# Performance work log

Hardware: AMD Instinct MI355X
Metric: run time of the kernel (lower is better)

## Reference

```python
import jax, jax.numpy as jnp
from jax import lax
import numpy as np

KSIZE = 3      # matching patch size
RATE = 2       # down/up-sampling rate
STRIDE = 1
FUSE_K = 3     # diagonal fuse kernel (identity eye(3))
SCALE = 10.0   # softmax_scale


def same_pad(H, k, s):
    out = -(-H // s)
    pt = max((out - 1) * s + k - H, 0)
    return (pt // 2, pt - pt // 2)


def extract_patches(x, k, s):
    # x: [C,H,W] -> patches [L, C, k, k] with TF 'SAME' padding (matches torch extract_image_patches)
    C, H, W = x.shape
    ph = same_pad(H, k, s)
    pw = same_pad(W, k, s)
    xp = jnp.pad(x, ((0, 0), ph, pw))
    Hp, Wp = xp.shape[1], xp.shape[2]
    Ho = (Hp - k) // s + 1
    Wo = (Wp - k) // s + 1
    sl = [xp[:, i:i + (Ho - 1) * s + 1:s, j:j + (Wo - 1) * s + 1:s]
          for i in range(k) for j in range(k)]
    p = jnp.stack(sl, axis=1).reshape(C, k, k, Ho * Wo)  # [C,k,k,L]
    return p.transpose(3, 0, 1, 2)  # [L,C,k,k]


def diag_sum(t, k=FUSE_K):
    # conv2d with eye(k) kernel, SAME padding: out[p,q] = sum_d t[p+d-k//2, q+d-k//2]
    p0 = (k - 1) // 2
    p1 = k - 1 - p0
    tp = jnp.pad(t, ((p0, p1), (p0, p1)))
    H, W = t.shape
    return sum(tp[d:d + H, d:d + W] for d in range(k))


def attend_one(fi, bi):
    # fi, bi: [C,H,W] full resolution
    C, H, W = fi.shape
    kernel = 2 * RATE
    # patches for reconstruction, from full-res background
    raw_w = extract_patches(bi, kernel, RATE * STRIDE)  # [L,C,4,4]
    # nearest downsample by rate for matching
    fs = fi[:, ::RATE, ::RATE]
    bs = bi[:, ::RATE, ::RATE]
    Hs, Ws = fs.shape[1], fs.shape[2]
    L = Hs * Ws
    # matching patches from downscaled background, l2-normalized
    w = extract_patches(bs, KSIZE, STRIDE)  # [L,C,3,3]
    norm = jnp.sqrt(jnp.sum(w * w, axis=(1, 2, 3), keepdims=True))
    wn = (w / jnp.maximum(norm, 1e-4)).reshape(L, -1)  # [L, C*9]
    # correlation conv == im2col matmul: yi[l, q] = <patch_l(b), patch_q(f)>
    fp = extract_patches(fs, KSIZE, 1).reshape(L, -1)  # [HWf, C*9]
    yi = jnp.einsum('lp,qp->lq', wn, fp)  # [HWb, HWf]
    # fuse: propagate scores along diagonals in both orderings
    t = diag_sum(yi)
    t = t.reshape(Hs, Ws, Hs, Ws).transpose(1, 0, 3, 2).reshape(L, L)
    t = diag_sum(t)
    yi = t.reshape(Ws, Hs, Ws, Hs).transpose(1, 0, 3, 2).reshape(L, Hs, Ws)
    # softmax over background-patch axis
    att = jax.nn.softmax(yi * SCALE, axis=0)  # [L,Hs,Ws]
    # conv_transpose2d(att, raw_w, stride=2, padding=1) / 4  via overlap-add
    contrib = jnp.einsum('lhw,lcij->cijhw', att, raw_w)  # [C,4,4,Hs,Ws]
    buf = jnp.zeros((C, 2 * Hs + 2, 2 * Ws + 2), fi.dtype)
    for i in range(kernel):
        for j in range(kernel):
            buf = buf.at[:, i:i + 2 * Hs:2, j:j + 2 * Ws:2].add(contrib[:, i, j])
    return buf[:, 1:2 * Hs + 1, 1:2 * Ws + 1] / 4.0  # [C,H,W]


def conv3x3_elu(x, w, bias):
    y = lax.conv_general_dilated(x, w, (1, 1), [(1, 1), (1, 1)],
                                 dimension_numbers=('NCHW', 'OIHW', 'NCHW'))
    return jax.nn.elu(y + bias[None, :, None, None])


def setup_inputs() -> dict:
    key = jax.random.key(0)
    k1, k2, k3, k4 = jax.random.split(key, 4)
    B, C, H, W = 4, 128, 128, 128
    f = jax.random.normal(k1, (B, C, H, W), jnp.float32)
    b = jax.random.normal(k2, (B, C, H, W), jnp.float32)
    w1 = jax.random.normal(k3, (C, C, 3, 3), jnp.float32) * 0.02
    b1 = jnp.zeros((C,), jnp.float32)
    w2 = jax.random.normal(k4, (C, C, 3, 3), jnp.float32) * 0.02
    b2 = jnp.zeros((C,), jnp.float32)
    return {'f': f, 'b': b, 'w1': w1, 'b1': b1, 'w2': w2, 'b2': b2}


def reference(f, b, w1, b1, w2, b2):
    y = jax.vmap(attend_one)(f, b)  # [B,C,H,W]
    y = conv3x3_elu(y, w1, b1)
    y = conv3x3_elu(y, w2, b2)
    return y
```

## Files before the change

kernel.cpp:

```cpp
#include <hip/hip_runtime.h>
#include <math.h>

using u16 = unsigned short;
using u32 = unsigned int;
typedef _Float16 f16x8 __attribute__((ext_vector_type(8)));
typedef float    f32x4 __attribute__((ext_vector_type(4)));

union F16U { _Float16 h; u16 u; };
__device__ __forceinline__ u16 f2h(float f) { F16U x; x.h = (_Float16)f; return x.u; }
__device__ __forceinline__ float h2f(u16 v) { F16U x; x.u = v; return (float)x.h; }

__device__ __forceinline__ void gl16(const void* g, void* l) {
  __builtin_amdgcn_global_load_lds((const __attribute__((address_space(1))) void*)g,
                                   (__attribute__((address_space(3))) void*)l, 16, 0, 0);
}


__global__ void k_wperm(const float* __restrict__ w, u16* __restrict__ Wp) {
  int idx = blockIdx.x * 256 + threadIdx.x;
  if (idx < 147456) {
    int co = idx / 1152, r = idx - co * 1152, tap = r >> 7, ci = r & 127;
    Wp[idx] = f2h(w[((size_t)co * 128 + ci) * 9 + tap]);
  }
}

__global__ void k_extract(const float* __restrict__ fi, const float* __restrict__ bi,
                          u16* __restrict__ fh, u16* __restrict__ fl,
                          u16* __restrict__ bh, u16* __restrict__ bl) {
  __shared__ u16 lt[4][64][136];
  int ph = blockIdx.x, t = threadIdx.x;
  for (int it = 0; it < 32; ++it) {
    int idx = it * 256 + t;
    int c = idx >> 6, pw = idx & 63;
    int src = c * 16384 + (2 * ph) * 128 + 2 * pw;
    float vf = fi[src], vb = bi[src];
    u16 fhi = f2h(vf), flo = f2h(vf - h2f(fhi));
    u16 bhi = f2h(vb), blo = f2h(vb - h2f(bhi));
    lt[0][pw][c] = fhi; lt[1][pw][c] = flo; lt[2][pw][c] = bhi; lt[3][pw][c] = blo;
  }
  __syncthreads();
  for (int it = 0; it < 16; ++it) {
    int g = it * 256 + t;
    int arr = g >> 10, rem = g & 1023, pw = rem >> 4, slot = rem & 15;
    uint4 v = *(const uint4*)&lt[arr][pw][slot * 8];
    u16* o = (arr == 0) ? fh : (arr == 1) ? fl : (arr == 2) ? bh : bl;
    *(uint4*)&o[(size_t)(ph * 64 + pw) * 128 + slot * 8] = v;
  }
}

__global__ void k_norm(const u16* __restrict__ bh, const u16* __restrict__ bl,
                       float* __restrict__ nrm) {
  int wid = threadIdx.x >> 6, lane = threadIdx.x & 63;
  int l = blockIdx.x * 4 + wid;
  int lh = l >> 6, lw = l & 63;
  float s = 0.f;
#pragma unroll
  for (int dh = -1; dh <= 1; ++dh)
#pragma unroll
    for (int dw = -1; dw <= 1; ++dw) {
      int y = lh + dh, x = lw + dw;
      if ((u32)y < 64u && (u32)x < 64u) {
        int p = y * 64 + x;
        u32 h2 = *(const u32*)&bh[(size_t)p * 128 + lane * 2];
        u32 l2 = *(const u32*)&bl[(size_t)p * 128 + lane * 2];
        float v0 = h2f((u16)h2) + h2f((u16)l2);
        float v1 = h2f((u16)(h2 >> 16)) + h2f((u16)(l2 >> 16));
        s += v0 * v0 + v1 * v1;
      }
    }
#pragma unroll
  for (int off = 32; off; off >>= 1) s += __shfl_xor(s, off);
  if (lane == 0) nrm[l] = sqrtf(s);
}

__global__ __launch_bounds__(256) void k_rgemm(const u16* __restrict__ fh, const u16* __restrict__ fl,
                                               const u16* __restrict__ bh, const u16* __restrict__ bl,
                                               float* __restrict__ C) {
  __shared__ u16 lds[4 * 128 * 64];
  u16* Ah = lds; u16* Al = lds + 8192; u16* Bh = lds + 16384; u16* Bl = lds + 24576;
  int t = threadIdx.x, lane = t & 63, wid = t >> 6;
  int wm = (wid >> 1) * 64, wn = (wid & 1) * 64;
  int fr = lane & 15, kb = lane >> 4;
  int q0 = blockIdx.y * 128, l0 = blockIdx.x * 128;
  f32x4 acc[4][4] = {};
  for (int kt = 0; kt < 128; kt += 64) {
#pragma unroll
    for (int j = 0; j < 4; ++j) {
      int g = wid * 256 + j * 64 + lane;
      int row = g >> 3, s = (g & 7) ^ (row & 7);
      int co = kt + s * 8;
      size_t ldso = (size_t)(wid * 256 + j * 64) * 8;
      gl16(&fh[(size_t)(q0 + row) * 128 + co], Ah + ldso);
      gl16(&fl[(size_t)(q0 + row) * 128 + co], Al + ldso);
      gl16(&bh[(size_t)(l0 + row) * 128 + co], Bh + ldso);
      gl16(&bl[(size_t)(l0 + row) * 128 + co], Bl + ldso);
    }
    __syncthreads();
#pragma unroll
    for (int kf = 0; kf < 2; ++kf) {
      f16x8 ah[4], al4[4], bh4[4], bl4[4];
#pragma unroll
      for (int mi = 0; mi < 4; ++mi) {
        int row = wm + mi * 16 + fr;
        int off = row * 64 + ((kf * 4 + kb) ^ (row & 7)) * 8;
        ah[mi] = *(const f16x8*)&Ah[off];
        al4[mi] = *(const f16x8*)&Al[off];
      }
#pragma unroll
      for (int ni = 0; ni < 4; ++ni) {
        int row = wn + ni * 16 + fr;
        int off = row * 64 + ((kf * 4 + kb) ^ (row & 7)) * 8;
        bh4[ni] = *(const f16x8*)&Bh[off];
        bl4[ni] = *(const f16x8*)&Bl[off];
      }
#pragma unroll
      for (int mi = 0; mi < 4; ++mi)
#pragma unroll
        for (int ni = 0; ni < 4; ++ni) {
          acc[mi][ni] = __builtin_amdgcn_mfma_f32_16x16x32_f16(ah[mi], bh4[ni], acc[mi][ni], 0, 0, 0);
          acc[mi][ni] = __builtin_amdgcn_mfma_f32_16x16x32_f16(ah[mi], bl4[ni], acc[mi][ni], 0, 0, 0);
          acc[mi][ni] = __builtin_amdgcn_mfma_f32_16x16x32_f16(al4[mi], bh4[ni], acc[mi][ni], 0, 0, 0);
        }
    }
    __syncthreads();
  }
#pragma unroll
  for (int mi = 0; mi < 4; ++mi) {
    int qr = q0 + wm + mi * 16 + kb * 4;
#pragma unroll
    for (int ni = 0; ni < 4; ++ni) {
      int lc = l0 + wn + ni * 16 + fr;
#pragma unroll
      for (int r = 0; r < 4; ++r)
        C[(size_t)(qr + r) * 4096 + lc] = acc[mi][ni][r];
    }
  }
}

__global__ __launch_bounds__(256) void k_passA(const float* __restrict__ R, const float* __restrict__ nrm,
                                               float* __restrict__ Y0) {
  int idx0 = (blockIdx.x * 256 + threadIdx.x) * 4;
  int q = idx0 >> 12, l0 = idx0 & 4095;
  int qh = q >> 6, qw = q & 63, lh = l0 >> 6, lw0 = l0 & 63;
  float a0 = 0.f, a1 = 0.f, a2 = 0.f, a3 = 0.f;
#define TAPA(dh, dw)                                                                   \
  {                                                                                    \
    constexpr int s = (dh) * 64 + (dw);                                                \
    constexpr int r = s & 3;                                                           \
    bool ok = ((u32)(qh + (dh)) < 64u) && ((u32)(qw + (dw)) < 64u) &&                  \
              ((u32)(lh + (dh)) < 64u);                                                \
    int ab = idx0 + s * 4097 - r;                                                      \
    ab = ab < 0 ? 0 : (ab > 16777208 ? 16777208 : ab);                                 \
    float4 lo = *(const float4*)&R[ab], hi = *(const float4*)&R[ab + 4];               \
    float xx[8] = {lo.x, lo.y, lo.z, lo.w, hi.x, hi.y, hi.z, hi.w};                    \
    if (ok) {                                                                          \
      if ((u32)(lw0 + 0 + (dw)) < 64u) a0 += xx[r + 0];                                \
      if ((u32)(lw0 + 1 + (dw)) < 64u) a1 += xx[r + 1];                                \
      if ((u32)(lw0 + 2 + (dw)) < 64u) a2 += xx[r + 2];                                \
      if ((u32)(lw0 + 3 + (dw)) < 64u) a3 += xx[r + 3];                                \
    }                                                                                  \
  }
  TAPA(-1, -1) TAPA(-1, 0) TAPA(-1, 1)
  TAPA(0, -1)  TAPA(0, 0)  TAPA(0, 1)
  TAPA(1, -1)  TAPA(1, 0)  TAPA(1, 1)
#undef TAPA
  float4 nv = *(const float4*)&nrm[l0];
  float4 o;
  o.x = a0 / fmaxf(nv.x, 1e-4f);
  o.y = a1 / fmaxf(nv.y, 1e-4f);
  o.z = a2 / fmaxf(nv.z, 1e-4f);
  o.w = a3 / fmaxf(nv.w, 1e-4f);
  *(float4*)&Y0[idx0] = o;
}

__global__ __launch_bounds__(256) void k_pbsm(const float* __restrict__ T1, u16* __restrict__ att) {
  int q = blockIdx.x, t = threadIdx.x;
  int qh = q >> 6;
  bool qok = (qh >= 2 && qh <= 61);
  float v[16];
#pragma unroll
  for (int p = 0; p < 4; ++p) {
    int l0 = p * 1024 + t * 4;
    int idx0 = q * 4096 + l0;
    int lh = l0 >> 6;
    float a0 = 0.f, a1 = 0.f, a2 = 0.f, a3 = 0.f;
    if (qok && lh >= 2 && lh <= 61) {
#define TAPB(s_)                                                                       \
  {                                                                                    \
    constexpr int s = (s_);                                                            \
    constexpr int r = s & 3;                                                           \
    const float* pp = T1 + (idx0 + s * 4097 - r);                                      \
    float4 lo = *(const float4*)pp, hi = *(const float4*)(pp + 4);                     \
    float xx[8] = {lo.x, lo.y, lo.z, lo.w, hi.x, hi.y, hi.z, hi.w};                    \
    a0 += xx[r + 0]; a1 += xx[r + 1]; a2 += xx[r + 2]; a3 += xx[r + 3];                \
  }
      TAPB(-65) TAPB(-64) TAPB(-63)
      TAPB(-1)  TAPB(0)   TAPB(1)
      TAPB(63)  TAPB(64)  TAPB(65)
#undef TAPB
    } else {
      float oe[4];
#pragma unroll
      for (int e = 0; e < 4; ++e) {
        int l = l0 + e;
        int pl = ((l & 63) << 6) | (l >> 6);
        int pq = ((q & 63) << 6) | (q >> 6);
        float acc = 0.f;
#pragma unroll
        for (int e2 = -1; e2 <= 1; ++e2) {
          int pa = pl + e2, pb = pq + e2;
          if ((u32)pa < 4096u && (u32)pb < 4096u) {
            int a = ((pa & 63) << 6) | (pa >> 6);
            int bq = ((pb & 63) << 6) | (pb >> 6);
#pragma unroll
            for (int e1 = -1; e1 <= 1; ++e1) {
              int aa = a + e1, bb = bq + e1;
              if ((u32)aa < 4096u && (u32)bb < 4096u) acc += T1[(size_t)bb * 4096 + aa];
            }
          }
        }
        oe[e] = acc;
      }
      a0 = oe[0]; a1 = oe[1]; a2 = oe[2]; a3 = oe[3];
    }
    v[p * 4 + 0] = a0; v[p * 4 + 1] = a1; v[p * 4 + 2] = a2; v[p * 4 + 3] = a3;
  }
  float m = -3.4e38f;
#pragma unroll
  for (int i = 0; i < 16; ++i) m = fmaxf(m, v[i]);
#pragma unroll
  for (int off = 32; off; off >>= 1) m = fmaxf(m, __shfl_xor(m, off));
  __shared__ float redm[4], reds[4];
  int wid = t >> 6, lane = t & 63;
  if (lane == 0) redm[wid] = m;
  __syncthreads();
  m = fmaxf(fmaxf(redm[0], redm[1]), fmaxf(redm[2], redm[3]));
  float s = 0.f;
#pragma unroll
  for (int i = 0; i < 16; ++i) { v[i] = expf(10.f * (v[i] - m)); s += v[i]; }
#pragma unroll
  for (int off = 32; off; off >>= 1) s += __shfl_xor(s, off);
  if (lane == 0) reds[wid] = s;
  __syncthreads();
  s = reds[0] + reds[1] + reds[2] + reds[3];
  float inv = 1.f / s;
  u16* arow = att + (size_t)q * 4096;
#pragma unroll
  for (int p = 0; p < 4; ++p) {
    union { u16 h[4]; uint2 u; } pk;
    pk.h[0] = f2h(v[p * 4 + 0] * inv); pk.h[1] = f2h(v[p * 4 + 1] * inv);
    pk.h[2] = f2h(v[p * 4 + 2] * inv); pk.h[3] = f2h(v[p * 4 + 3] * inv);
    *(uint2*)&arow[p * 1024 + t * 4] = pk.u;
  }
}

__global__ void k_rwt(const float* __restrict__ bi, u16* __restrict__ RWt) {
  int tid = blockIdx.x * 256 + threadIdx.x;
  int m = tid >> 10, lq = (tid & 1023) * 4;
  int c = m >> 4, i = (m >> 2) & 3, j = m & 3;
  int y = 2 * (lq >> 6) - 1 + i;
  union { u16 h[4]; uint2 u; } pk;
#pragma unroll
  for (int e = 0; e < 4; ++e) {
    int x = 2 * ((lq + e) & 63) - 1 + j;
    float v = 0.f;
    if ((u32)y < 128u && (u32)x < 128u) v = bi[c * 16384 + y * 128 + x];
    pk.h[e] = f2h(v);
  }
  *(uint2*)&RWt[(size_t)m * 4096 + lq] = pk.u;
}

__global__ __launch_bounds__(256) void k_gemm_pv(const u16* __restrict__ A, const u16* __restrict__ Bt,
                                                 float* __restrict__ C) {
  __shared__ u16 lds[2 * 16384];
  int t = threadIdx.x, lane = t & 63, wid = t >> 6;
  int wm = (wid >> 1) * 64, wn = (wid & 1) * 64;
  int fr = lane & 15, kb = lane >> 4;
  int bid = blockIdx.x;
  int my = (bid & 7) * 4 + ((bid >> 3) & 3);
  int nx = bid >> 5;
  int m0 = my * 128, n0 = nx * 128;
  f32x4 acc[4][4] = {};
#define STAGE(buf, kt)                                                                  \
  {                                                                                     \
    u16* lA = lds + (buf) * 16384;                                                      \
    u16* lB = lA + 8192;                                                                \
    _Pragma("unroll")                                                                   \
    for (int j = 0; j < 4; ++j) {                                                       \
      int g = wid * 256 + j * 64 + lane;                                                \
      int row = g >> 3, sw = (g & 7) ^ (row & 7);                                       \
      size_t ldso = (size_t)(wid * 256 + j * 64) * 8;                                   \
      gl16(&A[(size_t)(m0 + row) * 4096 + (kt) + sw * 8], lA + ldso);                   \
      gl16(&Bt[(size_t)(n0 + row) * 4096 + (kt) + sw * 8], lB + ldso);                  \
    }                                                                                   \
  }
  STAGE(0, 0)
  __syncthreads();
  int cur = 0;
  for (int kt = 0; kt < 4096; kt += 64) {
    if (kt + 64 < 4096) STAGE(cur ^ 1, kt + 64)
    u16* la = lds + cur * 16384;
    u16* lb = la + 8192;
#pragma unroll
    for (int ks = 0; ks < 2; ++ks) {
      f16x8 af[4], bfr[4];
#pragma unroll
      for (int mi = 0; mi < 4; ++mi) {
        int row = wm + mi * 16 + fr;
        af[mi] = *(const f16x8*)&la[row * 64 + ((ks * 32 + kb * 8) ^ ((row & 7) << 3))];
      }
#pragma unroll
      for (int ni = 0; ni < 4; ++ni) {
        int row = wn + ni * 16 + fr;
        bfr[ni] = *(const f16x8*)&lb[row * 64 + ((ks * 32 + kb * 8) ^ ((row & 7) << 3))];
      }
#pragma unroll
      for (int mi = 0; mi < 4; ++mi)
#pragma unroll
        for (int ni = 0; ni < 4; ++ni)
          acc[mi][ni] = __builtin_amdgcn_mfma_f32_16x16x32_f16(af[mi], bfr[ni], acc[mi][ni], 0, 0, 0);
    }
    __syncthreads();
    cur ^= 1;
  }
#undef STAGE
#pragma unroll
  for (int mi = 0; mi < 4; ++mi) {
    int mr = m0 + wm + mi * 16 + kb * 4;
#pragma unroll
    for (int ni = 0; ni < 4; ++ni) {
      int nc = n0 + wn + ni * 16 + fr;
#pragma unroll
      for (int r = 0; r < 4; ++r)
        C[(size_t)(mr + r) * 2048 + nc] = acc[mi][ni][r];
    }
  }
}

__global__ void k_overlap(const float* __restrict__ O, u16* __restrict__ Yh) {
  int idx = blockIdx.x * 256 + threadIdx.x;
  int c = idx & 127, pix = idx >> 7;
  int ox = pix & 127, oy = pix >> 7;
  int py = oy + 1, px = ox + 1;
  float s = 0.f;
#pragma unroll
  for (int di = 0; di < 2; ++di) {
    int i = (py & 1) + 2 * di;
    int hs = (py - i) >> 1;
    if ((u32)hs >= 64u) continue;
#pragma unroll
    for (int dj = 0; dj < 2; ++dj) {
      int j = (px & 1) + 2 * dj;
      int wsx = (px - j) >> 1;
      if ((u32)wsx >= 64u) continue;
      s += O[(size_t)(hs * 64 + wsx) * 2048 + c * 16 + i * 4 + j];
    }
  }
  Yh[idx] = f2h(0.25f * s);
}

template<int OUT_F16>
__global__ __launch_bounds__(256) void k_conv(const u16* __restrict__ In, const u16* __restrict__ Wp,
                                              const float* __restrict__ bias, void* __restrict__ out_,
                                              const u16* __restrict__ zg) {
  __shared__ u16 lds[2 * 128 * 64];
  u16* la = lds; u16* lb = lds + 8192;
  int t = threadIdx.x, lane = t & 63, wid = t >> 6;
  int wm = (wid >> 1) * 64, wn = (wid & 1) * 64;
  int fr = lane & 15, kb = lane >> 4;
  int yrow = blockIdx.x, bidx = blockIdx.y;
  const u16* inH = In + (size_t)bidx * 2097152;
  f32x4 acc[4][4] = {};
  for (int step = 0; step < 18; ++step) {
    int tap = step >> 1, ci0 = (step & 1) * 64;
    int dy = tap / 3, dx = tap - 3 * (tap / 3);
    int y = yrow + dy - 1;
#pragma unroll
    for (int j = 0; j < 4; ++j) {
      int g = wid * 256 + j * 64 + lane;
      int row = g >> 3, s = (g & 7) ^ (row & 7);
      size_t ldso = (size_t)(wid * 256 + j * 64) * 8;
      gl16(&Wp[(size_t)row * 1152 + step * 64 + s * 8], la + ldso);
      int xx = row + dx - 1;
      const u16* src = ((u32)y < 128u && (u32)xx < 128u)
                         ? &inH[((size_t)y * 128 + xx) * 128 + ci0 + s * 8] : zg;
      gl16(src, lb + ldso);
    }
    __syncthreads();
#pragma unroll
    for (int ks = 0; ks < 2; ++ks) {
      f16x8 af[4], bfr[4];
#pragma unroll
      for (int mi = 0; mi < 4; ++mi) {
        int row = wm + mi * 16 + fr;
        af[mi] = *(const f16x8*)&la[row * 64 + ((ks * 32 + kb * 8) ^ ((row & 7) << 3))];
      }
#pragma unroll
      for (int ni = 0; ni < 4; ++ni) {
        int row = wn + ni * 16 + fr;
        bfr[ni] = *(const f16x8*)&lb[row * 64 + ((ks * 32 + kb * 8) ^ ((row & 7) << 3))];
      }
#pragma unroll
      for (int mi = 0; mi < 4; ++mi)
#pragma unroll
        for (int ni = 0; ni < 4; ++ni)
          acc[mi][ni] = __builtin_amdgcn_mfma_f32_16x16x32_f16(af[mi], bfr[ni], acc[mi][ni], 0, 0, 0);
    }
    __syncthreads();
  }
#pragma unroll
  for (int mi = 0; mi < 4; ++mi) {
    int co = wm + mi * 16 + kb * 4;
#pragma unroll
    for (int ni = 0; ni < 4; ++ni) {
      int x = wn + ni * 16 + fr;
      if (OUT_F16) {
        union { u16 h[4]; uint2 v; } pk;
#pragma unroll
        for (int r = 0; r < 4; ++r) {
          float val = acc[mi][ni][r] + bias[co + r];
          val = val > 0.f ? val : expm1f(val);
          pk.h[r] = f2h(val);
        }
        u16* oH = (u16*)out_ + (size_t)bidx * 2097152;
        *(uint2*)&oH[((size_t)yrow * 128 + x) * 128 + co] = pk.v;
      } else {
        float* oF = (float*)out_ + (size_t)bidx * 2097152;
#pragma unroll
        for (int r = 0; r < 4; ++r) {
          float val = acc[mi][ni][r] + bias[co + r];
          val = val > 0.f ? val : expm1f(val);
          oF[(size_t)(co + r) * 16384 + yrow * 128 + x] = val;
        }
      }
    }
  }
}


extern "C" void kernel_launch(void* const* d_in, const int* in_sizes, int n_in,
                              void* d_out, int out_size, void* d_ws, size_t ws_size,
                              hipStream_t stream) {
  const float* f  = (const float*)d_in[0];
  const float* b  = (const float*)d_in[1];
  const float* w1 = (const float*)d_in[2];
  const float* b1 = (const float*)d_in[3];
  const float* w2 = (const float*)d_in[4];
  const float* b2 = (const float*)d_in[5];
  float* out = (float*)d_out;
  char* ws = (char*)d_ws;

  float* S0   = (float*)(ws);
  float* S1   = (float*)(ws + 67108864);
  u16*   fsTh = (u16*)(ws + 134217728);
  u16*   fsTl = (u16*)(ws + 135266304);
  u16*   bsTh = (u16*)(ws + 136314880);
  u16*   bsTl = (u16*)(ws + 137363456);
  float* nrm  = (float*)(ws + 138412032);
  u16*   Yh   = (u16*)(ws + 138428416);
  u16*   Wp1  = (u16*)(ws + 155205632);
  u16*   Wp2  = (u16*)(ws + 155500544);
  u16*   att  = (u16*)S0;
  u16*   RWt  = (u16*)S1;
  float* O    = (float*)(ws + 67108864 + 16777216);
  u16*   Z1h  = (u16*)S0;
  u16*   zg   = (u16*)(ws + 50331648);

  k_wperm<<<576, 256, 0, stream>>>(w1, Wp1);
  k_wperm<<<576, 256, 0, stream>>>(w2, Wp2);

  for (int i = 0; i < 4; ++i) {
    const float* fb = f + (size_t)i * 2097152;
    const float* bb = b + (size_t)i * 2097152;
    k_extract<<<64, 256, 0, stream>>>(fb, bb, fsTh, fsTl, bsTh, bsTl);
    k_norm<<<1024, 256, 0, stream>>>(bsTh, bsTl, nrm);
    k_rgemm<<<dim3(32, 32), 256, 0, stream>>>(fsTh, fsTl, bsTh, bsTl, S0);
    k_passA<<<16384, 256, 0, stream>>>(S0, nrm, S1);
    k_pbsm<<<4096, 256, 0, stream>>>(S1, att);
    k_rwt<<<8192, 256, 0, stream>>>(bb, RWt);
    k_gemm_pv<<<512, 256, 0, stream>>>(att, RWt, O);
    k_overlap<<<8192, 256, 0, stream>>>(O, Yh + (size_t)i * 2097152);
  }

  hipMemsetAsync(zg, 0, 256, stream);
  k_conv<1><<<dim3(128, 4), 256, 0, stream>>>(Yh, Wp1, b1, Z1h, zg);
  k_conv<0><<<dim3(128, 4), 256, 0, stream>>>(Z1h, Wp2, b2, out, zg);

  (void)in_sizes; (void)n_in; (void)out_size; (void)ws_size;
}
```

Baseline: 1.122 ms.

## Remap block indices per XCD for L2 locality across score kernels

Block IDs in rgemm, passA, pbsm and overlap are remapped so consecutive blocks dispatched round-robin to the same XCD work on contiguous rows of the score matrix. The aim is to improve per-XCD L2 hit rates for the overlapping diagonal stencil reads of the 64MB score buffers. k_overlap also changes its thread-to-element mapping (channel-major iteration, strided writes) to match this scheme, which turns its f16 stores into scattered, non-coalesced writes.

Measured after the change: 1.072 ms. 4.5% less time.

```diff
diff --git a/kernel.cpp b/kernel.cpp
--- a/kernel.cpp
+++ b/kernel.cpp
@@ -81,7 +81,10 @@
   int t = threadIdx.x, lane = t & 63, wid = t >> 6;
   int wm = (wid >> 1) * 64, wn = (wid & 1) * 64;
   int fr = lane & 15, kb = lane >> 4;
-  int q0 = blockIdx.y * 128, l0 = blockIdx.x * 128;
+  int b = blockIdx.x;
+  int xcd = b & 7, r = b >> 3;
+  int by = xcd * 4 + (r & 3), bx = r >> 2;
+  int q0 = by * 128, l0 = bx * 128;
   f32x4 acc[4][4] = {};
   for (int kt = 0; kt < 128; kt += 64) {
 #pragma unroll
@@ -131,33 +134,37 @@
     for (int ni = 0; ni < 4; ++ni) {
       int lc = l0 + wn + ni * 16 + fr;
 #pragma unroll
-      for (int r = 0; r < 4; ++r)
-        C[(size_t)(qr + r) * 4096 + lc] = acc[mi][ni][r];
+      for (int r2 = 0; r2 < 4; ++r2)
+        C[(size_t)(qr + r2) * 4096 + lc] = acc[mi][ni][r2];
     }
   }
 }
 
 __global__ __launch_bounds__(256) void k_passA(const float* __restrict__ R, const float* __restrict__ nrm,
                                                float* __restrict__ Y0) {
-  int idx0 = (blockIdx.x * 256 + threadIdx.x) * 4;
-  int q = idx0 >> 12, l0 = idx0 & 4095;
+  int b = blockIdx.x;
+  int xcd = b & 7, r = b >> 3;
+  int q = xcd * 512 + (r >> 2);
+  int part = r & 3;
+  int l0 = part * 1024 + threadIdx.x * 4;
+  int idx0 = q * 4096 + l0;
   int qh = q >> 6, qw = q & 63, lh = l0 >> 6, lw0 = l0 & 63;
   float a0 = 0.f, a1 = 0.f, a2 = 0.f, a3 = 0.f;
 #define TAPA(dh, dw)                                                                   \
   {                                                                                    \
     constexpr int s = (dh) * 64 + (dw);                                                \
-    constexpr int r = s & 3;                                                           \
+    constexpr int rr = s & 3;                                                          \
     bool ok = ((u32)(qh + (dh)) < 64u) && ((u32)(qw + (dw)) < 64u) &&                  \
               ((u32)(lh + (dh)) < 64u);                                                \
-    int ab = idx0 + s * 4097 - r;                                                      \
+    int ab = idx0 + s * 4097 - rr;                                                     \
     ab = ab < 0 ? 0 : (ab > 16777208 ? 16777208 : ab);                                 \
     float4 lo = *(const float4*)&R[ab], hi = *(const float4*)&R[ab + 4];               \
     float xx[8] = {lo.x, lo.y, lo.z, lo.w, hi.x, hi.y, hi.z, hi.w};                    \
     if (ok) {                                                                          \
-      if ((u32)(lw0 + 0 + (dw)) < 64u) a0 += xx[r + 0];                                \
-      if ((u32)(lw0 + 1 + (dw)) < 64u) a1 += xx[r + 1];                                \
-      if ((u32)(lw0 + 2 + (dw)) < 64u) a2 += xx[r + 2];                                \
-      if ((u32)(lw0 + 3 + (dw)) < 64u) a3 += xx[r + 3];                                \
+      if ((u32)(lw0 + 0 + (dw)) < 64u) a0 += xx[rr + 0];                               \
+      if ((u32)(lw0 + 1 + (dw)) < 64u) a1 += xx[rr + 1];                               \
+      if ((u32)(lw0 + 2 + (dw)) < 64u) a2 += xx[rr + 2];                               \
+      if ((u32)(lw0 + 3 + (dw)) < 64u) a3 += xx[rr + 3];                               \
     }                                                                                  \
   }
   TAPA(-1, -1) TAPA(-1, 0) TAPA(-1, 1)
@@ -174,7 +181,9 @@
 }
 
 __global__ __launch_bounds__(256) void k_pbsm(const float* __restrict__ T1, u16* __restrict__ att) {
-  int q = blockIdx.x, t = threadIdx.x;
+  int b = blockIdx.x;
+  int q = (b & 7) * 512 + (b >> 3);
+  int t = threadIdx.x;
   int qh = q >> 6;
   bool qok = (qh >= 2 && qh <= 61);
   float v[16];
@@ -188,11 +197,11 @@
 #define TAPB(s_)                                                                       \
   {                                                                                    \
     constexpr int s = (s_);                                                            \
-    constexpr int r = s & 3;                                                           \
-    const float* pp = T1 + (idx0 + s * 4097 - r);                                      \
+    constexpr int rr = s & 3;                                                          \
+    const float* pp = T1 + (idx0 + s * 4097 - rr);                                     \
     float4 lo = *(const float4*)pp, hi = *(const float4*)(pp + 4);                     \
     float xx[8] = {lo.x, lo.y, lo.z, lo.w, hi.x, hi.y, hi.z, hi.w};                    \
-    a0 += xx[r + 0]; a1 += xx[r + 1]; a2 += xx[r + 2]; a3 += xx[r + 3];                \
+    a0 += xx[rr + 0]; a1 += xx[rr + 1]; a2 += xx[rr + 2]; a3 += xx[rr + 3];            \
   }
       TAPB(-65) TAPB(-64) TAPB(-63)
       TAPB(-1)  TAPB(0)   TAPB(1)
@@ -338,9 +347,13 @@
 }
 
 __global__ void k_overlap(const float* __restrict__ O, u16* __restrict__ Yh) {
-  int idx = blockIdx.x * 256 + threadIdx.x;
-  int c = idx & 127, pix = idx >> 7;
-  int ox = pix & 127, oy = pix >> 7;
+  int b = blockIdx.x;
+  int xcd = b & 7, r = b >> 3;
+  int oypair = xcd * 8 + (r & 7);
+  int c = r >> 3;
+  int t = threadIdx.x;
+  int idx = c * 16384 + oypair * 256 + t;
+  int ox = idx & 127, oy = (idx & 16383) >> 7;
   int py = oy + 1, px = ox + 1;
   float s = 0.f;
 #pragma unroll
@@ -356,7 +369,7 @@
       s += O[(size_t)(hs * 64 + wsx) * 2048 + c * 16 + i * 4 + j];
     }
   }
-  Yh[idx] = f2h(0.25f * s);
+  Yh[((size_t)oy * 128 + ox) * 128 + c] = f2h(0.25f * s);
 }
 
 template<int OUT_F16>
@@ -474,7 +487,7 @@
     const float* bb = b + (size_t)i * 2097152;
     k_extract<<<64, 256, 0, stream>>>(fb, bb, fsTh, fsTl, bsTh, bsTl);
     k_norm<<<1024, 256, 0, stream>>>(bsTh, bsTl, nrm);
-    k_rgemm<<<dim3(32, 32), 256, 0, stream>>>(fsTh, fsTl, bsTh, bsTl, S0);
+    k_rgemm<<<1024, 256, 0, stream>>>(fsTh, fsTl, bsTh, bsTl, S0);
     k_passA<<<16384, 256, 0, stream>>>(S0, nrm, S1);
     k_pbsm<<<4096, 256, 0, stream>>>(S1, att);
     k_rwt<<<8192, 256, 0, stream>>>(bb, RWt);
```
